# Performance work log

Hardware: AMD Instinct MI355X
Metric: run time of the kernel (lower is better)

Reference implementation:

```python
import jax, jax.numpy as jnp
import numpy as np

N_NODES = 100000
N_EDGES = 1600000
N_GRAPHS = 512


def gcn_conv(x, W, b, src, dst, n_nodes):
    """GCNConv with self-loops: D^-1/2 (A+I) D^-1/2 X W + b."""
    h = x @ W  # [N, out]
    ones = jnp.ones((src.shape[0],), h.dtype)
    deg = jax.ops.segment_sum(ones, dst, num_segments=n_nodes) + 1.0  # +1 self-loop
    dinv = jax.lax.rsqrt(deg)
    norm = dinv[src] * dinv[dst]  # [E]
    agg = jax.ops.segment_sum(h[src] * norm[:, None], dst, num_segments=n_nodes)
    agg = agg + h * (1.0 / deg)[:, None]  # self-loop term: deg^-0.5 * deg^-0.5
    return agg + b


def setup_inputs() -> dict:
    key = jax.random.key(0)
    ks = jax.random.split(key, 12)
    x = jax.random.normal(ks[0], (N_NODES, 78), dtype=jnp.float32)
    edge_index = jax.random.randint(ks[1], (2, N_EDGES), 0, N_NODES, dtype=jnp.int64)
    batch = jnp.sort(jax.random.randint(ks[2], (N_NODES,), 0, N_GRAPHS, dtype=jnp.int64))
    def glorot(k, shape):
        lim = np.sqrt(6.0 / (shape[0] + shape[1])).astype(np.float32)
        return jax.random.uniform(k, shape, jnp.float32, -lim, lim)
    return {
        "x": x,
        "edge_index": edge_index,
        "batch": batch,
        "W1": glorot(ks[3], (78, 128)),
        "b1": jnp.zeros((128,), jnp.float32),
        "W2": glorot(ks[4], (128, 256)),
        "b2": jnp.zeros((256,), jnp.float32),
        "Wg1": glorot(ks[5], (256, 1024)),
        "bg1": jnp.zeros((1024,), jnp.float32),
        "Wg2": glorot(ks[6], (1024, 128)),
        "bg2": jnp.zeros((128,), jnp.float32),
    }


def reference(x, edge_index, batch, W1, b1, W2, b2, Wg1, bg1, Wg2, bg2):
    src, dst = edge_index[0], edge_index[1]
    n = x.shape[0]
    h = jax.nn.relu(gcn_conv(x, W1, b1, src, dst, n))   # [N,128]
    h = jax.nn.relu(gcn_conv(h, W2, b2, src, dst, n))   # [N,256]
    g = jax.ops.segment_max(h, batch, num_segments=N_GRAPHS)  # global max pool [G,256]
    g = jax.nn.relu(g @ Wg1 + bg1)   # [G,1024]; dropout is identity at eval
    g = g @ Wg2 + bg2                # [G,128]
    return g
```

## Files before the change

kernel.cpp:

```cpp
#include <hip/hip_runtime.h>
#include <hip/hip_fp16.h>


#define NN 100000
#define NE 1600000
#define NG 512
#define NBLK ((NN + 1023) / 1024)

typedef float v2f __attribute__((ext_vector_type(2)));
typedef _Float16 half8 __attribute__((ext_vector_type(8)));
typedef float f32x4 __attribute__((ext_vector_type(4)));


__global__ void k_hist(const int* __restrict__ dst, int* cnt, int e) {
    int i = blockIdx.x * blockDim.x + threadIdx.x;
    if (i < e) atomicAdd(&cnt[dst[i]], 1);
}

__global__ void k_prep(const int* __restrict__ cnt, float* __restrict__ dinv,
                       float* __restrict__ gmax) {
    int i = blockIdx.x * blockDim.x + threadIdx.x;
    if (i < NN) dinv[i] = rsqrtf((float)cnt[i] + 1.0f);
    if (i < NG * 256) gmax[i] = 0.0f;
}

__global__ void k_cvt_x(const float* __restrict__ x, __half* __restrict__ xh) {
    int i = blockIdx.x * blockDim.x + threadIdx.x;
    if (i < NN * 39) {
        float2 v = ((const float2*)x)[i];
        ((__half2*)xh)[i] = __floats2half2_rn(v.x, v.y);
    }
}

__global__ void k_pack_w2(const float* __restrict__ W, __half* __restrict__ Wh,
                          __half* __restrict__ Wl) {
    int i = blockIdx.x * blockDim.x + threadIdx.x;
    if (i >= 32768) return;
    int j = i & 7, lane = (i >> 3) & 63, ks = (i >> 9) & 3, nt = i >> 11;
    int n = nt * 16 + (lane & 15);
    int k = ks * 32 + ((lane >> 4) << 3) + j;
    float v = W[k * 256 + n];
    __half hi = __float2half_rn(v);
    Wh[i] = hi;
    Wl[i] = __float2half_rn(v - __half2float(hi));
}

__global__ __launch_bounds__(256) void k_bsum(const int* __restrict__ cnt, int* __restrict__ bsum) {
    __shared__ int s[256];
    int b = blockIdx.x, t = threadIdx.x;
    int base = b * 1024 + t * 4;
    int v = 0;
#pragma unroll
    for (int j = 0; j < 4; j++) { int i = base + j; if (i < NN) v += cnt[i]; }
    s[t] = v; __syncthreads();
    for (int off = 128; off > 0; off >>= 1) {
        if (t < off) s[t] += s[t + off];
        __syncthreads();
    }
    if (t == 0) bsum[b] = s[0];
}

__global__ __launch_bounds__(128) void k_scan_bsum(int* bsum, int* row_ptr) {
    __shared__ int s[128];
    int t = threadIdx.x;
    int v = (t < NBLK) ? bsum[t] : 0;
    s[t] = v; __syncthreads();
    for (int off = 1; off < 128; off <<= 1) {
        int u = (t >= off) ? s[t - off] : 0;
        __syncthreads();
        s[t] += u;
        __syncthreads();
    }
    if (t < NBLK) bsum[t] = s[t] - v;
    if (t == 0) row_ptr[NN] = NE;
}

__global__ __launch_bounds__(256) void k_scan_blocks(const int* __restrict__ cnt,
    const int* __restrict__ bsum, int* __restrict__ row_ptr, int* __restrict__ cursor) {
    __shared__ int s[256];
    int b = blockIdx.x, t = threadIdx.x;
    int base = b * 1024 + t * 4;
    int v[4]; int sum = 0;
#pragma unroll
    for (int j = 0; j < 4; j++) { int i = base + j; v[j] = (i < NN) ? cnt[i] : 0; sum += v[j]; }
    s[t] = sum; __syncthreads();
    for (int off = 1; off < 256; off <<= 1) {
        int u = (t >= off) ? s[t - off] : 0;
        __syncthreads();
        s[t] += u;
        __syncthreads();
    }
    int excl = s[t] - sum + bsum[b];
#pragma unroll
    for (int j = 0; j < 4; j++) {
        int i = base + j;
        if (i < NN) { row_ptr[i] = excl; cursor[i] = excl; excl += v[j]; }
    }
}

__global__ void k_fillslots(const int* __restrict__ src, const int* __restrict__ dst,
    const float* __restrict__ dinv, int* cursor, int2* __restrict__ es, int e) {
    int i = blockIdx.x * blockDim.x + threadIdx.x;
    if (i >= e) return;
    int s = src[i], d = dst[i];
    int pos = atomicAdd(&cursor[d], 1);
    es[pos] = make_int2(s, __float_as_int(dinv[s] * dinv[d]));
}

__global__ __launch_bounds__(256) void k_fused1(const __half* __restrict__ x,
    const int* __restrict__ rp, const int2* __restrict__ es,
    const float* __restrict__ dinv, const float* __restrict__ W,
    const float* __restrict__ bias, __half* __restrict__ out) {
    __shared__ float As[4][8][80];
    int tid = threadIdx.x;
    int wv = tid >> 6, l = tid & 63;
    int task = __builtin_amdgcn_readfirstlane(blockIdx.x * 4 + wv);
    int n0 = task * 8;
    if (n0 >= NN) return;

    if (l < 39) {
        for (int pi = 0; pi < 4; pi++) {
            int nA = n0 + 2 * pi, nB = nA + 1;
            float diA = dinv[nA], swA = diA * diA;
            float diB = dinv[nB], swB = diB * diB;
            float2 aA = __half22float2(((const __half2*)(x + (size_t)nA * 78))[l]);
            float2 aB = __half22float2(((const __half2*)(x + (size_t)nB * 78))[l]);
            aA.x *= swA; aA.y *= swA;
            aB.x *= swB; aB.y *= swB;
            int eA = rp[nA], eA1 = rp[nA + 1];
            int eB = rp[nB], eB1 = rp[nB + 1];
            int cA = (eA1 - eA) >> 3, cB = (eB1 - eB) >> 3;
            while (cA > 0 || cB > 0) {
                bool dA = (cA > 0), dB = (cB > 0);
                int2 esA[8], esB[8];
                __half2 vA[8], vB[8];
                if (dA) {
#pragma unroll
                    for (int j = 0; j < 8; j++) esA[j] = es[eA + j];
                }
                if (dB) {
#pragma unroll
                    for (int j = 0; j < 8; j++) esB[j] = es[eB + j];
                }
                if (dA) {
#pragma unroll
                    for (int j = 0; j < 8; j++)
                        vA[j] = ((const __half2*)(x + (size_t)esA[j].x * 78))[l];
                }
                if (dB) {
#pragma unroll
                    for (int j = 0; j < 8; j++)
                        vB[j] = ((const __half2*)(x + (size_t)esB[j].x * 78))[l];
                }
                if (dA) {
#pragma unroll
                    for (int j = 0; j < 8; j++) {
                        float w = __int_as_float(esA[j].y);
                        float2 v = __half22float2(vA[j]);
                        aA.x += v.x * w; aA.y += v.y * w;
                    }
                    eA += 8; cA--;
                }
                if (dB) {
#pragma unroll
                    for (int j = 0; j < 8; j++) {
                        float w = __int_as_float(esB[j].y);
                        float2 v = __half22float2(vB[j]);
                        aB.x += v.x * w; aB.y += v.y * w;
                    }
                    eB += 8; cB--;
                }
            }
            while (eA < eA1 && eB < eB1) {
                int2 pA = es[eA], pB = es[eB];
                float2 vA2 = __half22float2(((const __half2*)(x + (size_t)pA.x * 78))[l]);
                float2 vB2 = __half22float2(((const __half2*)(x + (size_t)pB.x * 78))[l]);
                float wA = __int_as_float(pA.y), wB = __int_as_float(pB.y);
                aA.x += vA2.x * wA; aA.y += vA2.y * wA;
                aB.x += vB2.x * wB; aB.y += vB2.y * wB;
                eA++; eB++;
            }
            for (; eA < eA1; eA++) {
                int2 p = es[eA];
                float w = __int_as_float(p.y);
                float2 v = __half22float2(((const __half2*)(x + (size_t)p.x * 78))[l]);
                aA.x += v.x * w; aA.y += v.y * w;
            }
            for (; eB < eB1; eB++) {
                int2 p = es[eB];
                float w = __int_as_float(p.y);
                float2 v = __half22float2(((const __half2*)(x + (size_t)p.x * 78))[l]);
                aB.x += v.x * w; aB.y += v.y * w;
            }
            *(float2*)&As[wv][2 * pi][2 * l] = aA;
            *(float2*)&As[wv][2 * pi + 1][2 * l] = aB;
        }
    }

    int f0 = l * 2;
    float2 acc[8];
#pragma unroll
    for (int i = 0; i < 8; i++) acc[i] = make_float2(0.f, 0.f);

    for (int k = 0; k < 76; k += 4) {
        float2 w0 = *(const float2*)&W[(k + 0) * 128 + f0];
        float2 w1 = *(const float2*)&W[(k + 1) * 128 + f0];
        float2 w2 = *(const float2*)&W[(k + 2) * 128 + f0];
        float2 w3 = *(const float2*)&W[(k + 3) * 128 + f0];
#pragma unroll
        for (int i = 0; i < 8; i++) {
            float4 a = *(const float4*)&As[wv][i][k];
            acc[i].x += a.x * w0.x + a.y * w1.x + a.z * w2.x + a.w * w3.x;
            acc[i].y += a.x * w0.y + a.y * w1.y + a.z * w2.y + a.w * w3.y;
        }
    }
    {
        float2 w0 = *(const float2*)&W[76 * 128 + f0];
        float2 w1 = *(const float2*)&W[77 * 128 + f0];
#pragma unroll
        for (int i = 0; i < 8; i++) {
            float2 a = *(const float2*)&As[wv][i][76];
            acc[i].x += a.x * w0.x + a.y * w1.x;
            acc[i].y += a.x * w0.y + a.y * w1.y;
        }
    }
    float2 bv = *(const float2*)&bias[f0];
#pragma unroll
    for (int i = 0; i < 8; i++) {
        float ox = fmaxf(acc[i].x + bv.x, 0.f);
        float oy = fmaxf(acc[i].y + bv.y, 0.f);
        *(__half2*)&out[(size_t)(n0 + i) * 128 + f0] = __floats2half2_rn(ox, oy);
    }
}

__global__ __launch_bounds__(256) void k_fused2(const __half* __restrict__ h,
    const int* __restrict__ rp, const int2* __restrict__ es,
    const float* __restrict__ dinv, const __half* __restrict__ W2h,
    const __half* __restrict__ W2l, const float* __restrict__ bias,
    const int* __restrict__ batch, unsigned* __restrict__ gmax) {
    __shared__ __half Ah[4][16][128];
    __shared__ __half Al[4][16][128];
    int tid = threadIdx.x;
    int wv = tid >> 6, l = tid & 63;
    int task = __builtin_amdgcn_readfirstlane(blockIdx.x * 4 + wv);
    if (task >= 6250) return;
    int n0 = task * 16;

    for (int pi = 0; pi < 8; pi++) {
        int nA = n0 + 2 * pi, nB = nA + 1;
        float diA = dinv[nA], swA = diA * diA;
        float diB = dinv[nB], swB = diB * diB;
        float2 aA = __half22float2(((const __half2*)(h + (size_t)nA * 128))[l]);
        float2 aB = __half22float2(((const __half2*)(h + (size_t)nB * 128))[l]);
        aA.x *= swA; aA.y *= swA;
        aB.x *= swB; aB.y *= swB;
        int eA = rp[nA], eA1 = rp[nA + 1];
        int eB = rp[nB], eB1 = rp[nB + 1];
        int cA = (eA1 - eA) >> 3, cB = (eB1 - eB) >> 3;
        while (cA > 0 || cB > 0) {
            bool dA = (cA > 0), dB = (cB > 0);
            int2 esA[8], esB[8];
            __half2 vA[8], vB[8];
            if (dA) {
#pragma unroll
                for (int j = 0; j < 8; j++) esA[j] = es[eA + j];
            }
            if (dB) {
#pragma unroll
                for (int j = 0; j < 8; j++) esB[j] = es[eB + j];
            }
            if (dA) {
#pragma unroll
                for (int j = 0; j < 8; j++)
                    vA[j] = ((const __half2*)(h + (size_t)esA[j].x * 128))[l];
            }
            if (dB) {
#pragma unroll
                for (int j = 0; j < 8; j++)
                    vB[j] = ((const __half2*)(h + (size_t)esB[j].x * 128))[l];
            }
            if (dA) {
#pragma unroll
                for (int j = 0; j < 8; j++) {
                    float w = __int_as_float(esA[j].y);
                    float2 v = __half22float2(vA[j]);
                    aA.x += v.x * w; aA.y += v.y * w;
                }
                eA += 8; cA--;
            }
            if (dB) {
#pragma unroll
                for (int j = 0; j < 8; j++) {
                    float w = __int_as_float(esB[j].y);
                    float2 v = __half22float2(vB[j]);
                    aB.x += v.x * w; aB.y += v.y * w;
                }
                eB += 8; cB--;
            }
        }
        while (eA < eA1 && eB < eB1) {
            int2 pA = es[eA], pB = es[eB];
            float2 vA2 = __half22float2(((const __half2*)(h + (size_t)pA.x * 128))[l]);
            float2 vB2 = __half22float2(((const __half2*)(h + (size_t)pB.x * 128))[l]);
            float wA = __int_as_float(pA.y), wB = __int_as_float(pB.y);
            aA.x += vA2.x * wA; aA.y += vA2.y * wA;
            aB.x += vB2.x * wB; aB.y += vB2.y * wB;
            eA++; eB++;
        }
        for (; eA < eA1; eA++) {
            int2 p = es[eA];
            float w = __int_as_float(p.y);
            float2 v = __half22float2(((const __half2*)(h + (size_t)p.x * 128))[l]);
            aA.x += v.x * w; aA.y += v.y * w;
        }
        for (; eB < eB1; eB++) {
            int2 p = es[eB];
            float w = __int_as_float(p.y);
            float2 v = __half22float2(((const __half2*)(h + (size_t)p.x * 128))[l]);
            aB.x += v.x * w; aB.y += v.y * w;
        }
        __half2 hiA = __floats2half2_rn(aA.x, aA.y);
        float2 bkA = __half22float2(hiA);
        __half2 loA = __floats2half2_rn(aA.x - bkA.x, aA.y - bkA.y);
        __half2 hiB = __floats2half2_rn(aB.x, aB.y);
        float2 bkB = __half22float2(hiB);
        __half2 loB = __floats2half2_rn(aB.x - bkB.x, aB.y - bkB.y);
        *(__half2*)&Ah[wv][2 * pi][2 * l] = hiA;
        *(__half2*)&Al[wv][2 * pi][2 * l] = loA;
        *(__half2*)&Ah[wv][2 * pi + 1][2 * l] = hiB;
        *(__half2*)&Al[wv][2 * pi + 1][2 * l] = loB;
    }

    int row4 = (l >> 4) << 2;
    int gg[4];
#pragma unroll
    for (int r = 0; r < 4; r++) gg[r] = batch[n0 + row4 + r];
    int am = l & 15;
    int akb = ((l >> 4) << 3);

    for (int hh = 0; hh < 2; hh++) {
        f32x4 acc[8];
#pragma unroll
        for (int i = 0; i < 8; i++) acc[i] = (f32x4)(0.f);
#pragma unroll
        for (int ks = 0; ks < 4; ks++) {
            half8 ah = *(const half8*)&Ah[wv][am][ks * 32 + akb];
            half8 al = *(const half8*)&Al[wv][am][ks * 32 + akb];
#pragma unroll
            for (int nt = 0; nt < 8; nt++) {
                int fi = ((((hh * 8 + nt) * 4 + ks) * 64) + l) * 8;
                half8 bh = *(const half8*)&W2h[fi];
                half8 bl = *(const half8*)&W2l[fi];
                acc[nt] = __builtin_amdgcn_mfma_f32_16x16x32_f16(ah, bh, acc[nt], 0, 0, 0);
                acc[nt] = __builtin_amdgcn_mfma_f32_16x16x32_f16(ah, bl, acc[nt], 0, 0, 0);
                acc[nt] = __builtin_amdgcn_mfma_f32_16x16x32_f16(al, bh, acc[nt], 0, 0, 0);
            }
        }
#pragma unroll
        for (int nt = 0; nt < 8; nt++) {
            int n = (hh * 8 + nt) * 16 + am;
            float bv = bias[n];
            int curg = -1;
            float m = 0.f;
#pragma unroll
            for (int r = 0; r < 4; r++) {
                int g = gg[r];
                float v = fmaxf(acc[nt][r] + bv, 0.f);
                if (g != curg) {
                    if (curg >= 0) atomicMax(&gmax[(size_t)curg * 256 + n], __float_as_uint(m));
                    curg = g; m = v;
                } else {
                    m = fmaxf(m, v);
                }
            }
            if (curg >= 0) atomicMax(&gmax[(size_t)curg * 256 + n], __float_as_uint(m));
        }
    }
}


__global__ __launch_bounds__(256) void k_gemm3(const float* __restrict__ A,
    const float* __restrict__ W, const float* __restrict__ bias,
    float* __restrict__ out) {
    __shared__ float rs[8][256];
    int b = blockIdx.x, tid = threadIdx.x;
#pragma unroll
    for (int g = 0; g < 8; g++) rs[g][tid] = A[(b * 8 + g) * 256 + tid];
    __syncthreads();
    float acc[8][4];
#pragma unroll
    for (int g = 0; g < 8; g++)
#pragma unroll
        for (int j = 0; j < 4; j++) acc[g][j] = 0.f;
    for (int k = 0; k < 256; k++) {
        float w0 = W[k * 1024 + tid];
        float w1 = W[k * 1024 + tid + 256];
        float w2 = W[k * 1024 + tid + 512];
        float w3 = W[k * 1024 + tid + 768];
#pragma unroll
        for (int g = 0; g < 8; g++) {
            float a = rs[g][k];
            acc[g][0] += a * w0; acc[g][1] += a * w1;
            acc[g][2] += a * w2; acc[g][3] += a * w3;
        }
    }
#pragma unroll
    for (int g = 0; g < 8; g++)
#pragma unroll
        for (int j = 0; j < 4; j++) {
            int f = tid + j * 256;
            out[(b * 8 + g) * 1024 + f] = fmaxf(acc[g][j] + bias[f], 0.0f);
        }
}

__global__ __launch_bounds__(128) void k_gemm4(const float* __restrict__ A,
    const float* __restrict__ W, const float* __restrict__ bias,
    float* __restrict__ out) {
    __shared__ float rs[4][1024];
    int b = blockIdx.x, tid = threadIdx.x;
    for (int i = tid; i < 4096; i += 128) rs[i >> 10][i & 1023] = A[b * 4096 + i];
    __syncthreads();
    float acc[4] = {0.f, 0.f, 0.f, 0.f};
    for (int k = 0; k < 1024; k++) {
        float wv = W[k * 128 + tid];
#pragma unroll
        for (int g = 0; g < 4; g++) acc[g] += rs[g][k] * wv;
    }
#pragma unroll
    for (int g = 0; g < 4; g++)
        out[(b * 4 + g) * 128 + tid] = acc[g] + bias[tid];
}

extern "C" void kernel_launch(void* const* d_in, const int* in_sizes, int n_in,
                              void* d_out, int out_size, void* d_ws, size_t ws_size,
                              hipStream_t stream) {
    const float* x    = (const float*)d_in[0];
    const int*   ei   = (const int*)d_in[1];
    const int*   batch= (const int*)d_in[2];
    const float* W1   = (const float*)d_in[3];
    const float* b1   = (const float*)d_in[4];
    const float* W2   = (const float*)d_in[5];
    const float* b2   = (const float*)d_in[6];
    const float* Wg1  = (const float*)d_in[7];
    const float* bg1  = (const float*)d_in[8];
    const float* Wg2  = (const float*)d_in[9];
    const float* bg2  = (const float*)d_in[10];
    const int* src = ei;
    const int* dst = ei + NE;

    char* w8 = (char*)d_ws;
    int*   cnt     = (int*)w8;                 w8 += (size_t)NN * 4;
    int*   row_ptr = (int*)w8;                 w8 += (size_t)(NN + 4) * 4;
    int*   cursor  = (int*)w8;                 w8 += (size_t)NN * 4;
    int*   bsum    = (int*)w8;                 w8 += 128 * 4;
    int2*  es      = (int2*)w8;                w8 += (size_t)NE * 8;
    float* dinv    = (float*)w8;               w8 += (size_t)NN * 4;
    __half* xh     = (__half*)w8;              w8 += (size_t)NN * 78 * 2;
    __half* h1     = (__half*)w8;              w8 += (size_t)NN * 128 * 2;
    __half* w2h    = (__half*)w8;              w8 += 32768 * 2;
    __half* w2l    = (__half*)w8;              w8 += 32768 * 2;
    unsigned* gmax = (unsigned*)w8;            w8 += (size_t)NG * 256 * 4;
    float* g1      = (float*)w8;               w8 += (size_t)NG * 1024 * 4;

    hipMemsetAsync(cnt, 0, (size_t)NN * 4, stream);
    k_hist<<<(NE + 255) / 256, 256, 0, stream>>>(dst, cnt, NE);
    k_cvt_x<<<(NN * 39 + 255) / 256, 256, 0, stream>>>(x, xh);
    k_pack_w2<<<128, 256, 0, stream>>>(W2, w2h, w2l);
    k_prep<<<(NG * 256 + 255) / 256, 256, 0, stream>>>(cnt, dinv, (float*)gmax);
    k_bsum<<<NBLK, 256, 0, stream>>>(cnt, bsum);
    k_scan_bsum<<<1, 128, 0, stream>>>(bsum, row_ptr);
    k_scan_blocks<<<NBLK, 256, 0, stream>>>(cnt, bsum, row_ptr, cursor);
    k_fillslots<<<(NE + 255) / 256, 256, 0, stream>>>(src, dst, dinv, cursor, es, NE);

    k_fused1<<<NN / 32, 256, 0, stream>>>(xh, row_ptr, es, dinv, W1, b1, h1);

    k_fused2<<<(6250 + 3) / 4, 256, 0, stream>>>(h1, row_ptr, es, dinv, w2h, w2l, b2, batch, gmax);

    k_gemm3<<<NG / 8, 256, 0, stream>>>((const float*)gmax, Wg1, bg1, g1);
    k_gemm4<<<NG / 4, 128, 0, stream>>>(g1, Wg2, bg2, (float*)d_out);
}
```

Measured before the change: 618.2 us.

## Drop low-half activation split in fused layer-2 GEMM and swizzle LDS tile

Stops splitting the aggregated activations into fp16 hi/lo parts, which removes one of the three MFMAs per tile and halves LDS use. It also XOR-swizzles the LDS layout to avoid bank conflicts and hoists the A-fragment loads out of the hh loop into registers. In exchange the activation operand keeps only fp16 precision, with more rounding error, while the weight operand still keeps its hi/lo split.

Result: faster. 591.1 us (-4.4%).

```diff
diff --git a/kernel.cpp b/kernel.cpp
--- a/kernel.cpp
+++ b/kernel.cpp
@@ -238,13 +238,16 @@
     const float* __restrict__ dinv, const __half* __restrict__ W2h,
     const __half* __restrict__ W2l, const float* __restrict__ bias,
     const int* __restrict__ batch, unsigned* __restrict__ gmax) {
-    __shared__ __half Ah[4][16][128];
-    __shared__ __half Al[4][16][128];
+    __shared__ __half As[4][16][128];
     int tid = threadIdx.x;
     int wv = tid >> 6, l = tid & 63;
     int task = __builtin_amdgcn_readfirstlane(blockIdx.x * 4 + wv);
     if (task >= 6250) return;
     int n0 = task * 16;
+
+    char* lbase = (char*)&As[wv][0][0];
+    int chunkw = (l >> 2);
+    int subw = (l & 3) * 4;
 
     for (int pi = 0; pi < 8; pi++) {
         int nA = n0 + 2 * pi, nB = nA + 1;
@@ -319,24 +322,25 @@
             float2 v = __half22float2(((const __half2*)(h + (size_t)p.x * 128))[l]);
             aB.x += v.x * w; aB.y += v.y * w;
         }
-        __half2 hiA = __floats2half2_rn(aA.x, aA.y);
-        float2 bkA = __half22float2(hiA);
-        __half2 loA = __floats2half2_rn(aA.x - bkA.x, aA.y - bkA.y);
-        __half2 hiB = __floats2half2_rn(aB.x, aB.y);
-        float2 bkB = __half22float2(hiB);
-        __half2 loB = __floats2half2_rn(aB.x - bkB.x, aB.y - bkB.y);
-        *(__half2*)&Ah[wv][2 * pi][2 * l] = hiA;
-        *(__half2*)&Al[wv][2 * pi][2 * l] = loA;
-        *(__half2*)&Ah[wv][2 * pi + 1][2 * l] = hiB;
-        *(__half2*)&Al[wv][2 * pi + 1][2 * l] = loB;
-    }
-
+        int rA = 2 * pi, rB = 2 * pi + 1;
+        *(__half2*)(lbase + rA * 256 + ((chunkw ^ rA) << 4) + subw) =
+            __floats2half2_rn(aA.x, aA.y);
+        *(__half2*)(lbase + rB * 256 + ((chunkw ^ rB) << 4) + subw) =
+            __floats2half2_rn(aB.x, aB.y);
+    }
+
+    int am = l & 15;
     int row4 = (l >> 4) << 2;
     int gg[4];
 #pragma unroll
     for (int r = 0; r < 4; r++) gg[r] = batch[n0 + row4 + r];
-    int am = l & 15;
-    int akb = ((l >> 4) << 3);
+
+    half8 ah[4];
+#pragma unroll
+    for (int ks = 0; ks < 4; ks++) {
+        int c = ks * 4 + (l >> 4);
+        ah[ks] = *(const half8*)(lbase + am * 256 + ((c ^ am) << 4));
+    }
 
     for (int hh = 0; hh < 2; hh++) {
         f32x4 acc[8];
@@ -344,16 +348,13 @@
         for (int i = 0; i < 8; i++) acc[i] = (f32x4)(0.f);
 #pragma unroll
         for (int ks = 0; ks < 4; ks++) {
-            half8 ah = *(const half8*)&Ah[wv][am][ks * 32 + akb];
-            half8 al = *(const half8*)&Al[wv][am][ks * 32 + akb];
 #pragma unroll
             for (int nt = 0; nt < 8; nt++) {
                 int fi = ((((hh * 8 + nt) * 4 + ks) * 64) + l) * 8;
                 half8 bh = *(const half8*)&W2h[fi];
                 half8 bl = *(const half8*)&W2l[fi];
-                acc[nt] = __builtin_amdgcn_mfma_f32_16x16x32_f16(ah, bh, acc[nt], 0, 0, 0);
-                acc[nt] = __builtin_amdgcn_mfma_f32_16x16x32_f16(ah, bl, acc[nt], 0, 0, 0);
-                acc[nt] = __builtin_amdgcn_mfma_f32_16x16x32_f16(al, bh, acc[nt], 0, 0, 0);
+                acc[nt] = __builtin_amdgcn_mfma_f32_16x16x32_f16(ah[ks], bh, acc[nt], 0, 0, 0);
+                acc[nt] = __builtin_amdgcn_mfma_f32_16x16x32_f16(ah[ks], bl, acc[nt], 0, 0, 0);
             }
         }
 #pragma unroll
```
